# Kernel tuning notes

Measured on AMD Instinct MI355X. Metric: run time of the kernel, lower is better.

Reference implementation:

```python
import jax, jax.numpy as jnp
import numpy as np

B, C, H, W = 8, 512, 32, 32
N_HEADS, HEAD_DIM = 8, 64
EPS = 1e-5


def _layernorm(x, g, b):
    mu = jnp.mean(x, axis=-1, keepdims=True)
    var = jnp.mean(jnp.square(x - mu), axis=-1, keepdims=True)
    return (x - mu) * jax.lax.rsqrt(var + EPS) * g + b


def setup_inputs() -> dict:
    key = jax.random.key(0)
    ks = jax.random.split(key, 16)
    u = lambda k, shp: jax.random.uniform(k, shp, dtype=jnp.float32)
    inp = {
        "x": jax.random.normal(ks[0], (B, C, H, W), dtype=jnp.float32),
        "t": jax.random.normal(ks[1], (B,), dtype=jnp.float32),
        # attention params (torch.rand init in source)
        "K_W": u(ks[2], (N_HEADS, C, HEAD_DIM)), "K_b": u(ks[3], (N_HEADS, HEAD_DIM)),
        "Q_W": u(ks[4], (N_HEADS, C, HEAD_DIM)), "Q_b": u(ks[5], (N_HEADS, HEAD_DIM)),
        "V_W": u(ks[6], (N_HEADS, C, HEAD_DIM)), "V_b": u(ks[7], (N_HEADS, HEAD_DIM)),
        "O_W": u(ks[8], (N_HEADS, HEAD_DIM, C)), "O_b": u(ks[9], (C,)),
        # pre-attention LayerNorm
        "ln1_g": jnp.ones((C,), jnp.float32), "ln1_b": jnp.zeros((C,), jnp.float32),
        # MLP: LayerNorm -> Linear -> GELU -> Linear
        "ln2_g": jnp.ones((C,), jnp.float32), "ln2_b": jnp.zeros((C,), jnp.float32),
        "W1": jax.random.normal(ks[10], (C, C), dtype=jnp.float32) / np.sqrt(C),
        "b1": jnp.zeros((C,), jnp.float32),
        "W2": jax.random.normal(ks[11], (C, C), dtype=jnp.float32) / np.sqrt(C),
        "b2": jnp.zeros((C,), jnp.float32),
    }
    return inp


def reference(x, t, K_W, K_b, Q_W, Q_b, V_W, V_b, O_W, O_b,
              ln1_g, ln1_b, ln2_g, ln2_b, W1, b1, W2, b2):
    b, c, h, w = x.shape
    xs = x.reshape(b, c, h * w).transpose(0, 2, 1)           # b s c
    res = _layernorm(xs, ln1_g, ln1_b)
    q = jnp.einsum('bsc,ncd->bsnd', res, Q_W) + Q_b          # b s n_h h_dim
    k = jnp.einsum('bsc,ncd->bsnd', res, K_W) + K_b
    v = jnp.einsum('bsc,ncd->bsnd', res, V_W) + V_b
    scores = jnp.einsum('bsnd,btnd->bnst', q, k) / jnp.sqrt(jnp.float32(c))
    attn = jax.nn.softmax(scores, axis=-1)                   # b n_h s s
    o = jnp.einsum('bnst,btnd->bsnd', attn, v)
    out = jnp.einsum('bsnd,ndc->bsc', o, O_W) + O_b
    out = out + xs                                           # residual
    m = _layernorm(out, ln2_g, ln2_b)
    m = jax.nn.gelu(m @ W1 + b1, approximate=False) @ W2 + b2
    out = m + out
    return out.transpose(0, 2, 1).reshape(b, c, h, w)
```

## Files before the change

kernel.cpp:

```cpp
#include <hip/hip_runtime.h>
#include <math.h>

#define BB 8
#define CC 512
#define SS 1024
#define NHH 8
#define HDD 64
#define KD 512

typedef __attribute__((ext_vector_type(8))) short short8;
typedef __attribute__((ext_vector_type(4))) float f32x4;
typedef __attribute__((ext_vector_type(4))) unsigned short ushort4v;

__device__ __forceinline__ unsigned short f2bf(float x) {
  union { float f; unsigned int u; } c; c.f = x;
  unsigned int r = (c.u + 0x7FFFu + ((c.u >> 16) & 1u)) >> 16;
  return (unsigned short)r;
}
__device__ __forceinline__ float b2f(unsigned short h) {
  union { unsigned int u; float f; } c; c.u = ((unsigned int)h) << 16; return c.f;
}

#define GLD_LDS(gp, lp) __builtin_amdgcn_global_load_lds( \
    (const __attribute__((address_space(1))) void*)(gp),  \
    (__attribute__((address_space(3))) void*)(lp), 16, 0, 0)

__device__ __forceinline__ float block_reduce_sum(float v) {
  __shared__ float sm[4];
  #pragma unroll
  for (int o = 32; o > 0; o >>= 1) v += __shfl_down(v, o, 64);
  if ((threadIdx.x & 63) == 0) sm[threadIdx.x >> 6] = v;
  __syncthreads();
  float r = (sm[0] + sm[1]) + (sm[2] + sm[3]);
  __syncthreads();
  return r;
}

__global__ __launch_bounds__(256) void ln1_apply(
    const float* __restrict__ x, const float2* __restrict__ mustd,
    const float* __restrict__ g, const float* __restrict__ be,
    unsigned short* __restrict__ yh, unsigned short* __restrict__ yl,
    unsigned short* __restrict__ xh, unsigned short* __restrict__ xl) {
  __shared__ float tile[32][33];
  const int b = blockIdx.z, c0 = blockIdx.y * 32, s0 = blockIdx.x * 32;
  const int tx = threadIdx.x, ty = threadIdx.y;
  const float* xb = x + ((size_t)b * CC + c0) * SS + s0;
  #pragma unroll
  for (int i = ty; i < 32; i += 8)
    tile[i][tx] = xb[(size_t)i * SS + tx];
  __syncthreads();
  const float gc = g[c0 + tx], bc = be[c0 + tx];
  #pragma unroll
  for (int i = ty; i < 32; i += 8) {
    const float2 ms = mustd[b * SS + s0 + i];
    const float v = tile[tx][i];
    const float y = (v - ms.x) * ms.y * gc + bc;
    const size_t oi = ((size_t)b * SS + s0 + i) * CC + c0 + tx;
    const unsigned short hy = f2bf(y);
    yh[oi] = hy; yl[oi] = f2bf(y - b2f(hy));
    const unsigned short hx = f2bf(v);
    xh[oi] = hx; xl[oi] = f2bf(v - b2f(hx));
  }
}

__global__ __launch_bounds__(256) void ln_bf16_k(const float* __restrict__ in,
                                                 const float* __restrict__ g,
                                                 const float* __restrict__ be,
                                                 unsigned short* __restrict__ outh) {
  size_t row = blockIdx.x;
  const float* r = in + row * CC;
  int t = threadIdx.x;
  float v0 = r[t], v1 = r[t + 256];
  float s = block_reduce_sum(v0 + v1);
  float mu = s * (1.0f / CC);
  float d0 = v0 - mu, d1 = v1 - mu;
  float vs = block_reduce_sum(d0 * d0 + d1 * d1);
  float rstd = rsqrtf(vs * (1.0f / CC) + 1e-5f);
  outh[row * CC + t]       = f2bf(d0 * rstd * g[t] + be[t]);
  outh[row * CC + t + 256] = f2bf(d1 * rstd * g[t + 256] + be[t + 256]);
}

__global__ __launch_bounds__(256) void convert_and_stats(
    const float* __restrict__ QW, const float* __restrict__ KW,
    const float* __restrict__ VW, const float* __restrict__ OW,
    const float* __restrict__ W1, const float* __restrict__ W2,
    const float* __restrict__ Qb, const float* __restrict__ Kb,
    const float* __restrict__ Vb,
    unsigned short* __restrict__ BtQKh, unsigned short* __restrict__ BtQKl,
    unsigned short* __restrict__ BtVh,
    unsigned short* __restrict__ BtOh, unsigned short* __restrict__ BtOl,
    unsigned short* __restrict__ BtW1h, unsigned short* __restrict__ BtW2h,
    float* __restrict__ qkvb,
    const float* __restrict__ x, float2* __restrict__ mustd) {
  const int bid = blockIdx.x;
  if (bid < 1536) {
    const float SCL = 0.044194173824159216f * 1.4426950408889634f;
    __shared__ float tile[32][33];
    const int bx = bid & 15, by = (bid >> 4) & 1, p = bid >> 5;
    const int wsel = p >> 3, sub = p & 7;
    const int k0 = bx * 32, d0 = by * 32;
    const int tx = threadIdx.x & 31, ty = threadIdx.x >> 5;
    const float* w; int rs; unsigned short *dh, *dl; int nbase; float mul = 1.0f;
    switch (wsel) {
      case 0:  w = QW + sub * 32768; rs = 64;  dh = BtQKh; dl = BtQKl;  nbase = sub * 64; mul = SCL; break;
      case 1:  w = KW + sub * 32768; rs = 64;  dh = BtQKh; dl = BtQKl;  nbase = 512 + sub * 64;  break;
      case 2:  w = VW + sub * 32768; rs = 64;  dh = BtVh;  dl = nullptr; nbase = sub * 64;       break;
      case 3:  w = OW + sub * 64;    rs = 512; dh = BtOh;  dl = BtOl;   nbase = sub * 64;        break;
      case 4:  w = W1 + sub * 64;    rs = 512; dh = BtW1h; dl = nullptr; nbase = sub * 64;       break;
      default: w = W2 + sub * 64;    rs = 512; dh = BtW2h; dl = nullptr; nbase = sub * 64;       break;
    }
    for (int i = ty; i < 32; i += 8)
      tile[i][tx] = w[(size_t)(k0 + i) * rs + d0 + tx];
    __syncthreads();
    for (int i = ty; i < 32; i += 8) {
      float f = tile[tx][i] * mul;
      unsigned short h = f2bf(f);
      size_t idx = (size_t)(nbase + d0 + i) * KD + k0 + tx;
      dh[idx] = h;
      if (dl) dl[idx] = f2bf(f - b2f(h));
    }
    if (bid == 0) {
      int t = threadIdx.x;
      for (int i = t; i < 1536; i += 256)
        qkvb[i] = i < 512 ? Qb[i] * SCL : (i < 1024 ? Kb[i - 512] : Vb[i - 1024]);
    }
  } else {
    const int bid2 = bid - 1536;
    const int b = bid2 >> 4, s0 = (bid2 & 15) * 64;
    const int sl = threadIdx.x & 63, cg = threadIdx.x >> 6;
    const float* xp = x + (size_t)b * CC * SS + s0 + sl;
    float ps = 0.f, pq = 0.f;
    #pragma unroll 8
    for (int i = 0; i < 128; ++i) {
      const float v = xp[(size_t)(cg * 128 + i) * SS];
      ps += v; pq += v * v;
    }
    __shared__ float sred[2][4][64];
    sred[0][cg][sl] = ps; sred[1][cg][sl] = pq;
    __syncthreads();
    if (cg == 0) {
      const float s = (sred[0][0][sl] + sred[0][1][sl]) + (sred[0][2][sl] + sred[0][3][sl]);
      const float q = (sred[1][0][sl] + sred[1][1][sl]) + (sred[1][2][sl] + sred[1][3][sl]);
      const float mu = s * (1.0f / CC);
      const float rs = rsqrtf(q * (1.0f / CC) - mu * mu + 1e-5f);
      mustd[b * SS + s0 + sl] = make_float2(mu, rs);
    }
  }
}

__global__ __launch_bounds__(256) void gemm_qkv(
    const unsigned short* __restrict__ Ah, const unsigned short* __restrict__ Al,
    const unsigned short* __restrict__ Bth, const unsigned short* __restrict__ Btl,
    const float* __restrict__ bias,
    unsigned short* __restrict__ qkh, unsigned short* __restrict__ qkl,
    unsigned short* __restrict__ vt) {
  __shared__ __align__(16) unsigned short smem[4 * 128 * 32];
  unsigned short* As = smem;
  unsigned short* Bs = smem + 2 * 128 * 32;
  const int tid = threadIdx.x;
  const int w = tid >> 6, l = tid & 63, quad = l >> 4, lm = l & 15;
  const int f = blockIdx.x, xcd = f & 7, gidx = f >> 3;
  const int n0 = (gidx >> 3) * 128;
  const int m0 = (((gidx & 7) << 3) | xcd) * 128;
  const bool splitB = n0 < 1024;
  const int wm = (w >> 1) * 64, wn = (w & 1) * 64;
  const int srow = tid >> 2;
  const int sch = (((tid & 3) ^ (srow & 3)) * 8);
  const unsigned short* Agh = Ah + (size_t)(m0 + srow) * KD + sch;
  const unsigned short* Agl = Al + (size_t)(m0 + srow) * KD + sch;
  const unsigned short* Bgh = Bth + (size_t)(n0 + srow) * KD + sch;
  const unsigned short* Bgl = Btl + (size_t)(n0 + srow) * KD + sch;
  unsigned short* Aswh = As + w * 512;
  unsigned short* Aswl = As + 4096 + w * 512;
  unsigned short* Bswh = Bs + w * 512;
  unsigned short* Bswl = Bs + 4096 + w * 512;
  const int rch = ((quad ^ (lm & 3)) * 8);
  const f32x4 fzero = {0.f, 0.f, 0.f, 0.f};
  f32x4 acc[4][4];
  #pragma unroll
  for (int i = 0; i < 4; ++i)
    #pragma unroll
    for (int j = 0; j < 4; ++j) acc[i][j] = fzero;
  for (int k0 = 0; k0 < KD; k0 += 32) {
    __syncthreads();
    GLD_LDS(Agh + k0, Aswh);
    GLD_LDS(Agh + k0 + 64 * KD, Aswh + 2048);
    GLD_LDS(Agl + k0, Aswl);
    GLD_LDS(Agl + k0 + 64 * KD, Aswl + 2048);
    GLD_LDS(Bgh + k0, Bswh);
    GLD_LDS(Bgh + k0 + 64 * KD, Bswh + 2048);
    if (splitB) {
      GLD_LDS(Bgl + k0, Bswl);
      GLD_LDS(Bgl + k0 + 64 * KD, Bswl + 2048);
    }
    __syncthreads();
    short8 afh[4], afl[4], bfh[4], bfl[4];
    #pragma unroll
    for (int i = 0; i < 4; ++i) {
      afh[i] = *(const short8*)(As + (wm + i * 16 + lm) * 32 + rch);
      afl[i] = *(const short8*)(As + 4096 + (wm + i * 16 + lm) * 32 + rch);
    }
    #pragma unroll
    for (int j = 0; j < 4; ++j)
      bfh[j] = *(const short8*)(Bs + (wn + j * 16 + lm) * 32 + rch);
    if (splitB) {
      #pragma unroll
      for (int j = 0; j < 4; ++j)
        bfl[j] = *(const short8*)(Bs + 4096 + (wn + j * 16 + lm) * 32 + rch);
      #pragma unroll
      for (int i = 0; i < 4; ++i)
        #pragma unroll
        for (int j = 0; j < 4; ++j) {
          f32x4 t = acc[i][j];
          t = __builtin_amdgcn_mfma_f32_16x16x32_bf16(afh[i], bfh[j], t, 0, 0, 0);
          t = __builtin_amdgcn_mfma_f32_16x16x32_bf16(afh[i], bfl[j], t, 0, 0, 0);
          t = __builtin_amdgcn_mfma_f32_16x16x32_bf16(afl[i], bfh[j], t, 0, 0, 0);
          acc[i][j] = t;
        }
    } else {
      #pragma unroll
      for (int i = 0; i < 4; ++i)
        #pragma unroll
        for (int j = 0; j < 4; ++j)
          acc[i][j] = __builtin_amdgcn_mfma_f32_16x16x32_bf16(afh[i], bfh[j], acc[i][j], 0, 0, 0);
    }
  }
  if (splitB) {
    #pragma unroll
    for (int i = 0; i < 4; ++i) {
      const int row = m0 + wm + i * 16 + quad * 4;
      #pragma unroll
      for (int j = 0; j < 4; ++j) {
        const int ncol = n0 + wn + j * 16 + lm;
        const float bv = bias[ncol];
        #pragma unroll
        for (int r = 0; r < 4; ++r) {
          const float xv = acc[i][j][r] + bv;
          const size_t oi = (size_t)(row + r) * 1024 + ncol;
          unsigned short h = f2bf(xv);
          qkh[oi] = h;
          qkl[oi] = f2bf(xv - b2f(h));
        }
      }
    }
  } else {
    __syncthreads();
    #pragma unroll
    for (int i = 0; i < 4; ++i) {
      const int mlb = wm + i * 16 + quad * 4;
      #pragma unroll
      for (int j = 0; j < 4; ++j) {
        const int nl = wn + j * 16 + lm;
        const float bv = bias[n0 + nl];
        ushort4v pk;
        #pragma unroll
        for (int r = 0; r < 4; ++r) pk[r] = f2bf(acc[i][j][r] + bv);
        const int chunk = ((mlb >> 3) ^ (nl & 15));
        *(ushort4v*)(smem + nl * 128 + chunk * 8 + (mlb & 7)) = pk;
      }
    }
    __syncthreads();
    const int tn = tid >> 4, tc = tid & 15;
    const int bb2 = m0 >> 10, sbase = m0 & 1023;
    #pragma unroll
    for (int pass = 0; pass < 8; ++pass) {
      const int nl = pass * 16 + tn;
      const int hh = (n0 - 1024 + nl) >> 6, dd = nl & 63;
      short8 v8 = *(const short8*)(smem + nl * 128 + ((tc ^ (nl & 15)) * 8));
      *(short8*)(vt + ((size_t)(bb2 * 8 + hh) * 64 + dd) * 1024 + sbase + tc * 8) = v8;
    }
  }
}

template<int SB, int GELU, int OUTMODE, int RESID, int TRANS>
__global__ __launch_bounds__(256) void gemm64(
    const unsigned short* __restrict__ Ah,
    const unsigned short* __restrict__ Bh, const unsigned short* __restrict__ Bl,
    const float* __restrict__ bias, const float* __restrict__ residf,
    const unsigned short* __restrict__ residh, const unsigned short* __restrict__ residl,
    unsigned short* __restrict__ outh, float* __restrict__ outf, int ldc) {
  constexpr int STAGE = (SB ? 3 : 2) * 8192;
  constexpr int TSIZE = TRANS ? 64 * 65 * 4 : 0;
  __shared__ __align__(16) unsigned char smem[STAGE > TSIZE ? STAGE : TSIZE];
  unsigned short* As  = (unsigned short*)smem;
  unsigned short* Bs  = (unsigned short*)(smem + 8192);
  unsigned short* Bls = (unsigned short*)(smem + 16384);
  float (*ttile)[65]  = (float(*)[65])smem;
  const int tid = threadIdx.x;
  const int w = tid >> 6, l = tid & 63, quad = l >> 4, lm = l & 15;
  const int f = blockIdx.x, xcd = f & 7, gidx = f >> 3;
  const int n0 = (gidx >> 4) * 64;
  const int m0 = (((gidx & 15) << 3) | xcd) * 64;
  const int wm = (w >> 1) * 32, wn = (w & 1) * 32;
  const int srow8 = tid >> 3;
  const int sch8  = ((tid & 7) ^ (srow8 & 7)) * 8;
  const unsigned short* Ag  = Ah + (size_t)(m0 + srow8) * KD + sch8;
  const unsigned short* Bg  = Bh + (size_t)(n0 + srow8) * KD + sch8;
  const unsigned short* Bgl = SB ? Bl + (size_t)(n0 + srow8) * KD + sch8 : nullptr;
  const f32x4 fzero = {0.f, 0.f, 0.f, 0.f};
  f32x4 acc[2][2];
  #pragma unroll
  for (int i = 0; i < 2; ++i)
    #pragma unroll
    for (int j = 0; j < 2; ++j) acc[i][j] = fzero;
  for (int k0 = 0; k0 < KD; k0 += 64) {
    __syncthreads();
    GLD_LDS(Ag + k0, As + w * 512);
    GLD_LDS(Ag + k0 + 32 * KD, As + 2048 + w * 512);
    GLD_LDS(Bg + k0, Bs + w * 512);
    GLD_LDS(Bg + k0 + 32 * KD, Bs + 2048 + w * 512);
    if constexpr (SB) {
      GLD_LDS(Bgl + k0, Bls + w * 512);
      GLD_LDS(Bgl + k0 + 32 * KD, Bls + 2048 + w * 512);
    }
    __syncthreads();
    #pragma unroll
    for (int ks = 0; ks < 2; ++ks) {
      const int kc = ((ks * 4 + quad) ^ (lm & 7)) * 8;
      short8 af[2], bfh[2], bfl[2];
      #pragma unroll
      for (int i = 0; i < 2; ++i)
        af[i] = *(const short8*)(As + (wm + i * 16 + lm) * 64 + kc);
      #pragma unroll
      for (int j = 0; j < 2; ++j)
        bfh[j] = *(const short8*)(Bs + (wn + j * 16 + lm) * 64 + kc);
      if constexpr (SB) {
        #pragma unroll
        for (int j = 0; j < 2; ++j)
          bfl[j] = *(const short8*)(Bls + (wn + j * 16 + lm) * 64 + kc);
      }
      #pragma unroll
      for (int i = 0; i < 2; ++i)
        #pragma unroll
        for (int j = 0; j < 2; ++j) {
          f32x4 t = acc[i][j];
          t = __builtin_amdgcn_mfma_f32_16x16x32_bf16(af[i], bfh[j], t, 0, 0, 0);
          if constexpr (SB)
            t = __builtin_amdgcn_mfma_f32_16x16x32_bf16(af[i], bfl[j], t, 0, 0, 0);
          acc[i][j] = t;
        }
    }
  }
  if constexpr (TRANS) __syncthreads();
  #pragma unroll
  for (int i = 0; i < 2; ++i) {
    const int row = m0 + wm + i * 16 + quad * 4;
    #pragma unroll
    for (int j = 0; j < 2; ++j) {
      const int col = n0 + wn + j * 16 + lm;
      const float bv = bias[col];
      #pragma unroll
      for (int r = 0; r < 4; ++r) {
        float x = acc[i][j][r] + bv;
        if (GELU) x = 0.5f * x * (1.0f + erff(x * 0.70710678118654752f));
        const size_t ri = (size_t)(row + r) * CC + col;
        if (RESID == 1) x += residf[ri];
        if (RESID == 2) x += b2f(residh[ri]) + b2f(residl[ri]);
        if constexpr (TRANS) {
          ttile[wm + i * 16 + quad * 4 + r][wn + j * 16 + lm] = x;
        } else {
          const size_t oi = (size_t)(row + r) * ldc + col;
          if (OUTMODE == 0) outf[oi] = x;
          else outh[oi] = f2bf(x);
        }
      }
    }
  }
  if constexpr (TRANS) {
    __syncthreads();
    const int bi = m0 >> 10, s0 = m0 & 1023;
    const int s = tid & 63;
    #pragma unroll
    for (int c0 = 0; c0 < 64; c0 += 4) {
      const int col = c0 + (tid >> 6);
      outf[(size_t)(bi * 512 + n0 + col) * 1024 + s0 + s] = ttile[s][col];
    }
  }
}

__global__ __launch_bounds__(256) void attn_mfma(
    const unsigned short* __restrict__ QKh, const unsigned short* __restrict__ QKl,
    const unsigned short* __restrict__ Vt, unsigned short* __restrict__ Oh) {
  __shared__ __align__(16) unsigned short Ksh[64 * 64], Ksl[64 * 64];
  __shared__ __align__(16) unsigned short Vts[64 * 64];
  __shared__ __align__(16) unsigned short Ps[4 * 16 * 88];
  const int f = blockIdx.x, xcd = f & 7, gidx = f >> 3;
  const int bh = (xcd << 3) | (gidx >> 4);
  const int q0 = (gidx & 15) * 64, h = bh & 7, b = bh >> 3;
  const int tid = threadIdx.x, w = tid >> 6, l = tid & 63, quad = l >> 4, lm = l & 15;
  const int LDQ = 2 * CC;
  const size_t qkbase = (size_t)b * SS * LDQ;
  const int srow8 = tid >> 3;
  const int sch8  = ((tid & 7) ^ (srow8 & 7)) * 8;
  const unsigned short* Vg = Vt + ((size_t)(b * 8 + h) * 64 + srow8) * 1024 + sch8;
  short8 qh[2], ql[2];
  {
    const size_t qo = qkbase + (size_t)(q0 + w * 16 + lm) * LDQ + h * 64 + quad * 8;
    qh[0] = *(const short8*)(QKh + qo);
    qh[1] = *(const short8*)(QKh + qo + 32);
    ql[0] = *(const short8*)(QKl + qo);
    ql[1] = *(const short8*)(QKl + qo + 32);
  }
  short8 bones;
  #pragma unroll
  for (int u = 0; u < 8; ++u) bones[u] = (lm == 0) ? (short)0x3F80 : (short)0;
  const f32x4 fzero = {0.f, 0.f, 0.f, 0.f};
  float mrow[4];
  f32x4 oacc[5];
  #pragma unroll
  for (int r = 0; r < 4; ++r) mrow[r] = -1e30f;
  #pragma unroll
  for (int j = 0; j < 5; ++j) oacc[j] = fzero;
  unsigned short* Pw = Ps + w * (16 * 88);
  for (int kt = 0; kt < SS; kt += 64) {
    __syncthreads();
    {
      const unsigned short* kg  = QKh + qkbase + (size_t)(kt + srow8) * LDQ + CC + h * 64 + sch8;
      const unsigned short* kgl = QKl + qkbase + (size_t)(kt + srow8) * LDQ + CC + h * 64 + sch8;
      GLD_LDS(kg, Ksh + w * 512);
      GLD_LDS(kg + 32 * LDQ, Ksh + 2048 + w * 512);
      GLD_LDS(kgl, Ksl + w * 512);
      GLD_LDS(kgl + 32 * LDQ, Ksl + 2048 + w * 512);
      GLD_LDS(Vg + kt, Vts + w * 512);
      GLD_LDS(Vg + kt + 32 * 1024, Vts + 2048 + w * 512);
    }
    __syncthreads();
    f32x4 sc[4];
    {
      const int kc = (quad ^ (lm & 7)) * 8;
      #pragma unroll
      for (int j = 0; j < 4; ++j) {
        short8 kh = *(const short8*)(Ksh + (j * 16 + lm) * 64 + kc);
        short8 kl = *(const short8*)(Ksl + (j * 16 + lm) * 64 + kc);
        f32x4 t = __builtin_amdgcn_mfma_f32_16x16x32_bf16(qh[0], kh, fzero, 0, 0, 0);
        t = __builtin_amdgcn_mfma_f32_16x16x32_bf16(qh[0], kl, t, 0, 0, 0);
        t = __builtin_amdgcn_mfma_f32_16x16x32_bf16(ql[0], kh, t, 0, 0, 0);
        sc[j] = t;
      }
    }
    {
      const int kc = ((4 + quad) ^ (lm & 7)) * 8;
      #pragma unroll
      for (int j = 0; j < 4; ++j) {
        short8 kh = *(const short8*)(Ksh + (j * 16 + lm) * 64 + kc);
        short8 kl = *(const short8*)(Ksl + (j * 16 + lm) * 64 + kc);
        f32x4 t = sc[j];
        t = __builtin_amdgcn_mfma_f32_16x16x32_bf16(qh[1], kh, t, 0, 0, 0);
        t = __builtin_amdgcn_mfma_f32_16x16x32_bf16(qh[1], kl, t, 0, 0, 0);
        t = __builtin_amdgcn_mfma_f32_16x16x32_bf16(ql[1], kh, t, 0, 0, 0);
        sc[j] = t;
      }
    }
    float mnew[4];
    bool chg = false;
    #pragma unroll
    for (int r = 0; r < 4; ++r) {
      float mt = fmaxf(fmaxf(sc[0][r], sc[1][r]), fmaxf(sc[2][r], sc[3][r]));
      #pragma unroll
      for (int mask = 1; mask < 16; mask <<= 1) mt = fmaxf(mt, __shfl_xor(mt, mask, 64));
      mnew[r] = fmaxf(mrow[r], mt);
      chg = chg || (mnew[r] > mrow[r]);
    }
    if (__any(chg)) {
      #pragma unroll
      for (int r = 0; r < 4; ++r) {
        const float alpha = exp2f(mrow[r] - mnew[r]);
        mrow[r] = mnew[r];
        #pragma unroll
        for (int j = 0; j < 5; ++j) oacc[j][r] *= alpha;
      }
    }
    #pragma unroll
    for (int r = 0; r < 4; ++r)
      #pragma unroll
      for (int j = 0; j < 4; ++j) sc[j][r] = exp2f(sc[j][r] - mrow[r]);
    #pragma unroll
    for (int r = 0; r < 4; ++r)
      #pragma unroll
      for (int j = 0; j < 4; ++j) {
        union { float f; unsigned int u; } pc; pc.f = sc[j][r];
        Pw[(quad * 4 + r) * 88 + j * 16 + lm] = (unsigned short)(pc.u >> 16);
      }
    #pragma unroll
    for (int st = 0; st < 2; ++st) {
      short8 ap = *(const short8*)(Pw + lm * 88 + st * 32 + quad * 8);
      const int kc = ((st * 4 + quad) ^ (lm & 7)) * 8;
      #pragma unroll
      for (int j = 0; j < 4; ++j) {
        short8 vv = *(const short8*)(Vts + (j * 16 + lm) * 64 + kc);
        oacc[j] = __builtin_amdgcn_mfma_f32_16x16x32_bf16(ap, vv, oacc[j], 0, 0, 0);
      }
      oacc[4] = __builtin_amdgcn_mfma_f32_16x16x32_bf16(ap, bones, oacc[4], 0, 0, 0);
    }
  }
  float inv[4];
  #pragma unroll
  for (int r = 0; r < 4; ++r) {
    const float lv = __shfl(oacc[4][r], l & 48, 64);
    inv[r] = 1.f / lv;
  }
  const size_t obase =
      (size_t)b * SS * CC + (size_t)(q0 + w * 16 + quad * 4) * CC + h * 64 + lm;
  #pragma unroll
  for (int j = 0; j < 4; ++j)
    #pragma unroll
    for (int r = 0; r < 4; ++r)
      Oh[obase + (size_t)r * CC + j * 16] = f2bf(oacc[j][r] * inv[r]);
}

extern "C" void kernel_launch(void* const* d_in, const int* in_sizes, int n_in,
                              void* d_out, int out_size, void* d_ws, size_t ws_size,
                              hipStream_t stream) {
  const float* x    = (const float*)d_in[0];
  const float* K_W  = (const float*)d_in[2];
  const float* K_b  = (const float*)d_in[3];
  const float* Q_W  = (const float*)d_in[4];
  const float* Q_b  = (const float*)d_in[5];
  const float* V_W  = (const float*)d_in[6];
  const float* V_b  = (const float*)d_in[7];
  const float* O_W  = (const float*)d_in[8];
  const float* O_b  = (const float*)d_in[9];
  const float* ln1g = (const float*)d_in[10];
  const float* ln1b = (const float*)d_in[11];
  const float* ln2g = (const float*)d_in[12];
  const float* ln2b = (const float*)d_in[13];
  const float* W1   = (const float*)d_in[14];
  const float* b1   = (const float*)d_in[15];
  const float* W2   = (const float*)d_in[16];
  const float* b2   = (const float*)d_in[17];
  float* out = (float*)d_out;

  unsigned char* ws = (unsigned char*)d_ws;
  const size_t MB = 1u << 20;
  unsigned short* qkh   = (unsigned short*)(ws);
  unsigned short* qkl   = (unsigned short*)(ws + 16 * MB);
  unsigned short* vt    = (unsigned short*)(ws + 32 * MB);
  unsigned short* ln1h  = (unsigned short*)(ws + 40 * MB);
  unsigned short* ln1l  = (unsigned short*)(ws + 48 * MB);
  unsigned short* xsh   = (unsigned short*)(ws + 56 * MB);
  unsigned short* xsl   = (unsigned short*)(ws + 64 * MB);
  unsigned short* oh    = ln1h;
  float* out1           = (float*)(ws + 72 * MB);
  unsigned short* ln2h  = qkh;
  unsigned short* geluh = (unsigned short*)(ws + 8 * MB);
  unsigned short* BtAll = (unsigned short*)(ws + 88 * MB);
  unsigned short* BtQKh = BtAll;
  unsigned short* BtVh  = BtAll + 1024 * 512;
  unsigned short* BtQKl = BtVh + 512 * 512;
  unsigned short* BtOh  = BtQKl + 1024 * 512;
  unsigned short* BtOl  = BtOh + 512 * 512;
  unsigned short* BtW1h = BtOl + 512 * 512;
  unsigned short* BtW2h = BtW1h + 512 * 512;
  float* qkvb           = (float*)(BtW2h + 512 * 512);
  float2* mustd         = (float2*)(ws + 96 * MB);

  dim3 tb32(32, 8);
  convert_and_stats<<<1536 + 128, 256, 0, stream>>>(
      Q_W, K_W, V_W, O_W, W1, W2, Q_b, K_b, V_b,
      BtQKh, BtQKl, BtVh, BtOh, BtOl, BtW1h, BtW2h, qkvb, x, mustd);
  ln1_apply<<<dim3(SS / 32, CC / 32, BB), tb32, 0, stream>>>(
      x, mustd, ln1g, ln1b, ln1h, ln1l, xsh, xsl);
  gemm_qkv<<<768, 256, 0, stream>>>(
      ln1h, ln1l, BtAll, BtQKl, qkvb, qkh, qkl, vt);
  attn_mfma<<<1024, 256, 0, stream>>>(qkh, qkl, vt, oh);
  gemm64<1, 0, 0, 2, 0><<<1024, 256, 0, stream>>>(
      oh, BtOh, BtOl, O_b, nullptr, xsh, xsl, nullptr, out1, CC);
  ln_bf16_k<<<BB * SS, 256, 0, stream>>>(out1, ln2g, ln2b, ln2h);
  gemm64<0, 1, 1, 0, 0><<<1024, 256, 0, stream>>>(
      ln2h, BtW1h, nullptr, b1, nullptr, nullptr, nullptr, geluh, nullptr, CC);
  gemm64<0, 0, 0, 1, 1><<<1024, 256, 0, stream>>>(
      geluh, BtW2h, nullptr, b2, out1, nullptr, nullptr, nullptr, out, CC);
}
```

Baseline: 271.3 us.

## Transpose attention MFMA operands so each lane owns one query row

Swaps the A/B operands of the QK^T and PV MFMAs so the score and output tiles are transposed, leaving each lane with a single query row. The row max then needs only two cross-lane shuffles instead of four per row. The extra MFMA against a ones vector that computed the softmax denominator is replaced by a lane-local running sum. P is packed to bf16 with byte perms and written to a swizzled LDS tile in 8-byte chunks, and the output is stored as 4-wide vectors instead of scalar bf16 writes.

```diff
diff --git a/kernel.cpp b/kernel.cpp
--- a/kernel.cpp
+++ b/kernel.cpp
@@ -11,6 +11,7 @@
 typedef __attribute__((ext_vector_type(8))) short short8;
 typedef __attribute__((ext_vector_type(4))) float f32x4;
 typedef __attribute__((ext_vector_type(4))) unsigned short ushort4v;
+typedef __attribute__((ext_vector_type(2))) unsigned int u32x2;
 
 __device__ __forceinline__ unsigned short f2bf(float x) {
   union { float f; unsigned int u; } c; c.f = x;
@@ -383,7 +384,7 @@
     const unsigned short* __restrict__ Vt, unsigned short* __restrict__ Oh) {
   __shared__ __align__(16) unsigned short Ksh[64 * 64], Ksl[64 * 64];
   __shared__ __align__(16) unsigned short Vts[64 * 64];
-  __shared__ __align__(16) unsigned short Ps[4 * 16 * 88];
+  __shared__ __align__(16) unsigned short Pts[4][16 * 64];
   const int f = blockIdx.x, xcd = f & 7, gidx = f >> 3;
   const int bh = (xcd << 3) | (gidx >> 4);
   const int q0 = (gidx & 15) * 64, h = bh & 7, b = bh >> 3;
@@ -401,17 +402,14 @@
     ql[0] = *(const short8*)(QKl + qo);
     ql[1] = *(const short8*)(QKl + qo + 32);
   }
-  short8 bones;
-  #pragma unroll
-  for (int u = 0; u < 8; ++u) bones[u] = (lm == 0) ? (short)0x3F80 : (short)0;
   const f32x4 fzero = {0.f, 0.f, 0.f, 0.f};
-  float mrow[4];
-  f32x4 oacc[5];
-  #pragma unroll
-  for (int r = 0; r < 4; ++r) mrow[r] = -1e30f;
-  #pragma unroll
-  for (int j = 0; j < 5; ++j) oacc[j] = fzero;
-  unsigned short* Pw = Ps + w * (16 * 88);
+  float m = -1e30f, lsum = 0.f;
+  f32x4 oacc[4];
+  #pragma unroll
+  for (int j = 0; j < 4; ++j) oacc[j] = fzero;
+  unsigned char* Pb = (unsigned char*)(Pts[w]);
+  const int pwbase = lm * 128 + ((quad & 1) << 3);
+  const int prbase = lm * 128;
   for (int kt = 0; kt < SS; kt += 64) {
     __syncthreads();
     {
@@ -432,9 +430,9 @@
       for (int j = 0; j < 4; ++j) {
         short8 kh = *(const short8*)(Ksh + (j * 16 + lm) * 64 + kc);
         short8 kl = *(const short8*)(Ksl + (j * 16 + lm) * 64 + kc);
-        f32x4 t = __builtin_amdgcn_mfma_f32_16x16x32_bf16(qh[0], kh, fzero, 0, 0, 0);
-        t = __builtin_amdgcn_mfma_f32_16x16x32_bf16(qh[0], kl, t, 0, 0, 0);
-        t = __builtin_amdgcn_mfma_f32_16x16x32_bf16(ql[0], kh, t, 0, 0, 0);
+        f32x4 t = __builtin_amdgcn_mfma_f32_16x16x32_bf16(kh, qh[0], fzero, 0, 0, 0);
+        t = __builtin_amdgcn_mfma_f32_16x16x32_bf16(kl, qh[0], t, 0, 0, 0);
+        t = __builtin_amdgcn_mfma_f32_16x16x32_bf16(kh, ql[0], t, 0, 0, 0);
         sc[j] = t;
       }
     }
@@ -445,67 +443,71 @@
         short8 kh = *(const short8*)(Ksh + (j * 16 + lm) * 64 + kc);
         short8 kl = *(const short8*)(Ksl + (j * 16 + lm) * 64 + kc);
         f32x4 t = sc[j];
-        t = __builtin_amdgcn_mfma_f32_16x16x32_bf16(qh[1], kh, t, 0, 0, 0);
-        t = __builtin_amdgcn_mfma_f32_16x16x32_bf16(qh[1], kl, t, 0, 0, 0);
-        t = __builtin_amdgcn_mfma_f32_16x16x32_bf16(ql[1], kh, t, 0, 0, 0);
+        t = __builtin_amdgcn_mfma_f32_16x16x32_bf16(kh, qh[1], t, 0, 0, 0);
+        t = __builtin_amdgcn_mfma_f32_16x16x32_bf16(kl, qh[1], t, 0, 0, 0);
+        t = __builtin_amdgcn_mfma_f32_16x16x32_bf16(kh, ql[1], t, 0, 0, 0);
         sc[j] = t;
       }
     }
-    float mnew[4];
-    bool chg = false;
-    #pragma unroll
-    for (int r = 0; r < 4; ++r) {
-      float mt = fmaxf(fmaxf(sc[0][r], sc[1][r]), fmaxf(sc[2][r], sc[3][r]));
-      #pragma unroll
-      for (int mask = 1; mask < 16; mask <<= 1) mt = fmaxf(mt, __shfl_xor(mt, mask, 64));
-      mnew[r] = fmaxf(mrow[r], mt);
-      chg = chg || (mnew[r] > mrow[r]);
-    }
-    if (__any(chg)) {
+    float mt0 = fmaxf(fmaxf(sc[0][0], sc[0][1]), fmaxf(sc[0][2], sc[0][3]));
+    float mt1 = fmaxf(fmaxf(sc[1][0], sc[1][1]), fmaxf(sc[1][2], sc[1][3]));
+    float mt2 = fmaxf(fmaxf(sc[2][0], sc[2][1]), fmaxf(sc[2][2], sc[2][3]));
+    float mt3 = fmaxf(fmaxf(sc[3][0], sc[3][1]), fmaxf(sc[3][2], sc[3][3]));
+    float mt = fmaxf(fmaxf(mt0, mt1), fmaxf(mt2, mt3));
+    mt = fmaxf(mt, __shfl_xor(mt, 16, 64));
+    mt = fmaxf(mt, __shfl_xor(mt, 32, 64));
+    const float mnew = fmaxf(m, mt);
+    if (__any(mnew > m)) {
+      const float alpha = exp2f(m - mnew);
+      m = mnew;
+      lsum *= alpha;
+      #pragma unroll
+      for (int j = 0; j < 4; ++j)
+        #pragma unroll
+        for (int r = 0; r < 4; ++r) oacc[j][r] *= alpha;
+    }
+    float ls = 0.f;
+    #pragma unroll
+    for (int j = 0; j < 4; ++j)
       #pragma unroll
       for (int r = 0; r < 4; ++r) {
-        const float alpha = exp2f(mrow[r] - mnew[r]);
-        mrow[r] = mnew[r];
-        #pragma unroll
-        for (int j = 0; j < 5; ++j) oacc[j][r] *= alpha;
-      }
-    }
-    #pragma unroll
-    for (int r = 0; r < 4; ++r)
-      #pragma unroll
-      for (int j = 0; j < 4; ++j) sc[j][r] = exp2f(sc[j][r] - mrow[r]);
-    #pragma unroll
-    for (int r = 0; r < 4; ++r)
-      #pragma unroll
-      for (int j = 0; j < 4; ++j) {
-        union { float f; unsigned int u; } pc; pc.f = sc[j][r];
-        Pw[(quad * 4 + r) * 88 + j * 16 + lm] = (unsigned short)(pc.u >> 16);
-      }
+        sc[j][r] = exp2f(sc[j][r] - m);
+        ls += sc[j][r];
+      }
+    ls += __shfl_xor(ls, 16, 64);
+    ls += __shfl_xor(ls, 32, 64);
+    lsum += ls;
+    #pragma unroll
+    for (int j = 0; j < 4; ++j) {
+      union { float f; unsigned int u; } c0, c1, c2, c3;
+      c0.f = sc[j][0]; c1.f = sc[j][1]; c2.f = sc[j][2]; c3.f = sc[j][3];
+      u32x2 pk;
+      pk[0] = __builtin_amdgcn_perm(c1.u, c0.u, 0x07060302u);
+      pk[1] = __builtin_amdgcn_perm(c3.u, c2.u, 0x07060302u);
+      const int slot = ((j << 1) | (quad >> 1)) ^ (lm & 7);
+      *(u32x2*)(Pb + pwbase + (slot << 4)) = pk;
+    }
     #pragma unroll
     for (int st = 0; st < 2; ++st) {
-      short8 ap = *(const short8*)(Pw + lm * 88 + st * 32 + quad * 8);
+      short8 pf = *(const short8*)(Pb + prbase + ((((st << 2) | quad) ^ (lm & 7)) << 4));
       const int kc = ((st * 4 + quad) ^ (lm & 7)) * 8;
       #pragma unroll
       for (int j = 0; j < 4; ++j) {
         short8 vv = *(const short8*)(Vts + (j * 16 + lm) * 64 + kc);
-        oacc[j] = __builtin_amdgcn_mfma_f32_16x16x32_bf16(ap, vv, oacc[j], 0, 0, 0);
-      }
-      oacc[4] = __builtin_amdgcn_mfma_f32_16x16x32_bf16(ap, bones, oacc[4], 0, 0, 0);
-    }
-  }
-  float inv[4];
-  #pragma unroll
-  for (int r = 0; r < 4; ++r) {
-    const float lv = __shfl(oacc[4][r], l & 48, 64);
-    inv[r] = 1.f / lv;
-  }
+        oacc[j] = __builtin_amdgcn_mfma_f32_16x16x32_bf16(vv, pf, oacc[j], 0, 0, 0);
+      }
+    }
+  }
+  const float inv = 1.f / lsum;
   const size_t obase =
-      (size_t)b * SS * CC + (size_t)(q0 + w * 16 + quad * 4) * CC + h * 64 + lm;
-  #pragma unroll
-  for (int j = 0; j < 4; ++j)
-    #pragma unroll
-    for (int r = 0; r < 4; ++r)
-      Oh[obase + (size_t)r * CC + j * 16] = f2bf(oacc[j][r] * inv[r]);
+      (size_t)b * SS * CC + (size_t)(q0 + w * 16 + lm) * CC + h * 64 + quad * 4;
+  #pragma unroll
+  for (int j = 0; j < 4; ++j) {
+    ushort4v pk;
+    #pragma unroll
+    for (int r = 0; r < 4; ++r) pk[r] = f2bf(oacc[j][r] * inv);
+    *(ushort4v*)(Oh + obase + j * 16) = pk;
+  }
 }
 
 extern "C" void kernel_launch(void* const* d_in, const int* in_sizes, int n_in,
```

Result: faster. 264.3 us (-2.6%).
